# Kernel optimization log

Hardware: AMD Instinct MI355X
Metric: run time of the kernel (lower is better)

Reference implementation:

```python
import jax, jax.numpy as jnp
import numpy as np

B, T, E, R, A, M = 64, 2000, 512, 1024, 512, 8


def setup_inputs() -> dict:
    key = jax.random.key(0)
    ks = jax.random.split(key, 9)
    attention_hidden_state = jax.random.normal(ks[0], (B, R), dtype=jnp.float32)
    memory = jax.random.normal(ks[1], (B, T, E), dtype=jnp.float32)
    previous_location = jax.random.uniform(ks[2], (B, 1, M), dtype=jnp.float32) * 10.0
    mask = jnp.zeros((B, T), dtype=bool)
    # F = Linear(R->A, bias, xavier tanh) -> Linear(A->A, no bias, xavier tanh) -> tanh -> lin(A->3M, bias)
    g = 5.0 / 3.0  # tanh gain
    lim1 = g * np.sqrt(6.0 / (R + A))
    W1 = jax.random.uniform(ks[3], (A, R), minval=-lim1, maxval=lim1, dtype=jnp.float32)
    b1 = jnp.zeros((A,), dtype=jnp.float32)
    lim2 = g * np.sqrt(6.0 / (A + A))
    W2 = jax.random.uniform(ks[4], (A, A), minval=-lim2, maxval=lim2, dtype=jnp.float32)
    lim3 = np.sqrt(1.0 / A)
    Wlin = jax.random.uniform(ks[5], (3 * M, A), minval=-lim3, maxval=lim3, dtype=jnp.float32) * 0.01
    blin = jax.random.uniform(ks[6], (3 * M,), minval=-lim3, maxval=lim3, dtype=jnp.float32) * 0.008 - 2.0
    return {"attention_hidden_state": attention_hidden_state, "memory": memory,
            "previous_location": previous_location, "mask": mask,
            "W1": W1, "b1": b1, "W2": W2, "Wlin": Wlin, "blin": blin}


def reference(attention_hidden_state, memory, previous_location, mask, W1, b1, W2, Wlin, blin):
    # normalize_attention_input=True
    h = jnp.tanh(attention_hidden_state)                       # (B, R)
    x = jnp.tanh((h @ W1.T + b1) @ W2.T)                       # (B, A) 2-layer variant
    y = (x @ Wlin.T + blin)[:, None, :]                        # (B, 1, 3M)
    m = y.shape[-1] // 3
    w, delta, scale = y[..., :m], y[..., m:2 * m], y[..., 2 * m:]
    delta = jax.nn.sigmoid(delta)                              # (B, 1, M)
    loc = previous_location + delta                            # (B, 1, M)
    scale = jax.nn.sigmoid(scale) * 2.0 + 1.0                  # (B, 1, M)
    pos = jnp.arange(memory.shape[1], dtype=memory.dtype)[None, :, None]  # (1, T, 1)
    d = loc - pos                                              # (B, T, M)
    z = 0.5 * (jax.lax.erf((d + 0.5) * scale) - jax.lax.erf((d - 0.5) * scale))
    wmix = jax.nn.sigmoid(w)[:, 0, :]                          # (B, M)
    alignment = jnp.einsum('btm,bm->bt', z, wmix)              # (B, T)
    alignment = jnp.where(mask, jnp.zeros((), alignment.dtype), alignment)  # score_mask_value=0
    attention_weights = jax.nn.softmax(alignment, axis=1)      # (B, T)
    attention_context = jnp.einsum('bt,bte->be', attention_weights, memory)  # (B, E)
    return attention_context, attention_weights, loc
```

## Files before the change

kernel.cpp:

```cpp
#include <hip/hip_runtime.h>
#include <math.h>

#define B 64
#define T 2000
#define E 512
#define R 1024
#define A 512
#define M 8

#define NCH 16
#define TCH (T / NCH)

__device__ __forceinline__ float sigmoidf_(float x) { return 1.0f / (1.0f + expf(-x)); }

__global__ __launch_bounds__(512) void mlp_align_kernel(
    const float* __restrict__ ahs, const float* __restrict__ prev_loc,
    const unsigned char* __restrict__ mask,
    const float* __restrict__ W1, const float* __restrict__ b1,
    const float* __restrict__ W2, const float* __restrict__ Wlin,
    const float* __restrict__ blin,
    float* __restrict__ out_w,
    float* __restrict__ out_loc)
{
    __shared__ float sh_h[R];
    __shared__ float sh_t[A];
    __shared__ float sh_x[A];
    __shared__ float sh_y[3 * M];
    __shared__ float sh_wmix[M], sh_loc[M], sh_scale[M];
    __shared__ float sred[8];
    __shared__ float sbval;

    const int b = blockIdx.x;
    const int tid = threadIdx.x;

    for (int k = tid; k < R; k += 512) sh_h[k] = tanhf(ahs[b * R + k]);
    __syncthreads();

    {
        const int j = tid;
        const float4* w4 = (const float4*)(W1 + (size_t)j * R);
        const float4* h4 = (const float4*)sh_h;
        float a0 = 0.f, a1 = 0.f, a2 = 0.f, a3 = 0.f;
#pragma unroll 4
        for (int k4 = 0; k4 < R / 4; k4 += 4) {
            float4 x0 = h4[k4 + 0], w0 = w4[k4 + 0];
            float4 x1 = h4[k4 + 1], w1 = w4[k4 + 1];
            float4 x2 = h4[k4 + 2], w2 = w4[k4 + 2];
            float4 x3 = h4[k4 + 3], w3 = w4[k4 + 3];
            a0 += x0.x * w0.x + x0.y * w0.y + x0.z * w0.z + x0.w * w0.w;
            a1 += x1.x * w1.x + x1.y * w1.y + x1.z * w1.z + x1.w * w1.w;
            a2 += x2.x * w2.x + x2.y * w2.y + x2.z * w2.z + x2.w * w2.w;
            a3 += x3.x * w3.x + x3.y * w3.y + x3.z * w3.z + x3.w * w3.w;
        }
        sh_t[j] = (a0 + a1) + (a2 + a3) + b1[j];
    }
    __syncthreads();

    {
        const int j = tid;
        const float4* w4 = (const float4*)(W2 + (size_t)j * A);
        const float4* t4 = (const float4*)sh_t;
        float a0 = 0.f, a1 = 0.f, a2 = 0.f, a3 = 0.f;
#pragma unroll 4
        for (int k4 = 0; k4 < A / 4; k4 += 4) {
            float4 x0 = t4[k4 + 0], w0 = w4[k4 + 0];
            float4 x1 = t4[k4 + 1], w1 = w4[k4 + 1];
            float4 x2 = t4[k4 + 2], w2 = w4[k4 + 2];
            float4 x3 = t4[k4 + 3], w3 = w4[k4 + 3];
            a0 += x0.x * w0.x + x0.y * w0.y + x0.z * w0.z + x0.w * w0.w;
            a1 += x1.x * w1.x + x1.y * w1.y + x1.z * w1.z + x1.w * w1.w;
            a2 += x2.x * w2.x + x2.y * w2.y + x2.z * w2.z + x2.w * w2.w;
            a3 += x3.x * w3.x + x3.y * w3.y + x3.z * w3.z + x3.w * w3.w;
        }
        sh_x[j] = tanhf((a0 + a1) + (a2 + a3));
    }
    __syncthreads();

    if (tid < 16 * 3 * M) {
        const int i = tid >> 4;
        const int lane = tid & 15;
        float s = 0.f;
        for (int k = lane; k < A; k += 16) s += sh_x[k] * Wlin[i * A + k];
        s += __shfl_down(s, 8, 16);
        s += __shfl_down(s, 4, 16);
        s += __shfl_down(s, 2, 16);
        s += __shfl_down(s, 1, 16);
        if (lane == 0) sh_y[i] = s + blin[i];
    }
    __syncthreads();

    if (tid < M) {
        const int m = tid;
        const float delta = sigmoidf_(sh_y[M + m]);
        const float loc = prev_loc[b * M + m] + delta;
        sh_wmix[m]  = sigmoidf_(sh_y[m]);
        sh_loc[m]   = loc;
        sh_scale[m] = sigmoidf_(sh_y[2 * M + m]) * 2.0f + 1.0f;
        out_loc[b * M + m] = loc;
    }
    __syncthreads();

    float a[4];
    float lmax = -1e30f;
#pragma unroll
    for (int i = 0; i < 4; ++i) {
        const int t = tid + i * 512;
        float v = 0.f;
        if (t < T) {
            const float tf = (float)t;
#pragma unroll
            for (int m = 0; m < M; ++m) {
                const float d = sh_loc[m] - tf;
                const float s = sh_scale[m];
                v += 0.5f * (erff((d + 0.5f) * s) - erff((d - 0.5f) * s)) * sh_wmix[m];
            }
            if (mask[b * T + t]) v = 0.f;
            lmax = fmaxf(lmax, v);
        }
        a[i] = v;
    }

    for (int off = 32; off > 0; off >>= 1) lmax = fmaxf(lmax, __shfl_down(lmax, off));
    if ((tid & 63) == 0) sred[tid >> 6] = lmax;
    __syncthreads();
    if (tid == 0) {
        float m0 = sred[0];
        for (int i = 1; i < 8; ++i) m0 = fmaxf(m0, sred[i]);
        sbval = m0;
    }
    __syncthreads();
    const float bmax = sbval;

    float lsum = 0.f;
#pragma unroll
    for (int i = 0; i < 4; ++i) {
        const int t = tid + i * 512;
        if (t < T) {
            a[i] = expf(a[i] - bmax);
            lsum += a[i];
        }
    }
    for (int off = 32; off > 0; off >>= 1) lsum += __shfl_down(lsum, off);
    if ((tid & 63) == 0) sred[tid >> 6] = lsum;
    __syncthreads();
    if (tid == 0) {
        float s0 = 0.f;
        for (int i = 0; i < 8; ++i) s0 += sred[i];
        sbval = s0;
    }
    __syncthreads();
    const float inv = 1.0f / sbval;

#pragma unroll
    for (int i = 0; i < 4; ++i) {
        const int t = tid + i * 512;
        if (t < T) out_w[b * T + t] = a[i] * inv;
    }
}

__global__ __launch_bounds__(512) void context_partial_kernel(
    const float* __restrict__ memory,
    const float* __restrict__ w,
    float* __restrict__ partials)
{
    __shared__ float sh_w[TCH];
    __shared__ float4 sh_acc[512];

    const int b = blockIdx.x;
    const int chunk = blockIdx.y;
    const int tid = threadIdx.x;
    const int t0 = chunk * TCH;

    if (tid < TCH) sh_w[tid] = w[b * T + t0 + tid];
    __syncthreads();

    const int e4 = tid & 127;
    const int tp = tid >> 7;
    const float4* mem4 = (const float4*)(memory + (size_t)(b * T + t0) * E);

    float4 acc = {0.f, 0.f, 0.f, 0.f};
#pragma unroll 4
    for (int t = tp; t < TCH; t += 4) {
        const float wv = sh_w[t];
        const float4 mv = mem4[(size_t)t * (E / 4) + e4];
        acc.x += wv * mv.x;
        acc.y += wv * mv.y;
        acc.z += wv * mv.z;
        acc.w += wv * mv.w;
    }
    sh_acc[tid] = acc;
    __syncthreads();

    if (tid < 128) {
        const float4 a0 = sh_acc[tid];
        const float4 a1 = sh_acc[tid + 128];
        const float4 a2 = sh_acc[tid + 256];
        const float4 a3 = sh_acc[tid + 384];
        float4 r;
        r.x = (a0.x + a1.x) + (a2.x + a3.x);
        r.y = (a0.y + a1.y) + (a2.y + a3.y);
        r.z = (a0.z + a1.z) + (a2.z + a3.z);
        r.w = (a0.w + a1.w) + (a2.w + a3.w);
        float4* dst = (float4*)(partials + ((size_t)b * NCH + chunk) * E);
        dst[tid] = r;
    }
}

__global__ __launch_bounds__(256) void context_reduce_kernel(
    const float* __restrict__ partials,
    float* __restrict__ out_ctx)
{
    const int idx = blockIdx.x * 256 + threadIdx.x;
    const int b = idx >> 9;
    const int e = idx & (E - 1);
    float s = 0.f;
#pragma unroll
    for (int c = 0; c < NCH; ++c) s += partials[((size_t)b * NCH + c) * E + e];
    out_ctx[idx] = s;
}

extern "C" void kernel_launch(void* const* d_in, const int* in_sizes, int n_in,
                              void* d_out, int out_size, void* d_ws, size_t ws_size,
                              hipStream_t stream) {
    const float* ahs      = (const float*)d_in[0];
    const float* memory   = (const float*)d_in[1];
    const float* prev_loc = (const float*)d_in[2];
    const unsigned char* mask = (const unsigned char*)d_in[3];
    const float* W1   = (const float*)d_in[4];
    const float* b1   = (const float*)d_in[5];
    const float* W2   = (const float*)d_in[6];
    const float* Wlin = (const float*)d_in[7];
    const float* blin = (const float*)d_in[8];

    float* out = (float*)d_out;
    float* out_ctx = out;
    float* out_w   = out + B * E;
    float* out_loc = out + B * E + B * T;
    float* partials = (float*)d_ws;

    mlp_align_kernel<<<dim3(B), dim3(512), 0, stream>>>(
        ahs, prev_loc, mask, W1, b1, W2, Wlin, blin, out_w, out_loc);

    context_partial_kernel<<<dim3(B, NCH), dim3(512), 0, stream>>>(
        memory, out_w, partials);

    context_reduce_kernel<<<dim3((B * E) / 256), dim3(256), 0, stream>>>(
        partials, out_ctx);
}
```

Before: 478.6 us.

## Coalesce MLP weight reads, drop softmax max pass, stream memory nontemporally

The MLP matvecs now use one wave per output row, so consecutive lanes read a row with coalesced float4 loads and a shuffle reduces it, replacing the strided per-thread row reads. The softmax max-subtraction pass and one block reduction are removed, since the alignment values are bounded mixture weights. The context partial kernel uses nontemporal loads and writes four partials per chunk without a shared-memory reduction, and the final reduce kernel is vectorised with float4 over 64 partials. Risks: skipping the max subtraction assumes small logits, and the workspace holds four times as many partials.

```diff
diff --git a/kernel.cpp b/kernel.cpp
--- a/kernel.cpp
+++ b/kernel.cpp
@@ -10,8 +10,14 @@
 
 #define NCH 16
 #define TCH (T / NCH)
+#define NP  (NCH * 4)
+
+typedef float nfloat4 __attribute__((ext_vector_type(4)));
 
 __device__ __forceinline__ float sigmoidf_(float x) { return 1.0f / (1.0f + expf(-x)); }
+__device__ __forceinline__ float dot4_(float4 a, float4 b) {
+    return (a.x * b.x + a.y * b.y) + (a.z * b.z + a.w * b.w);
+}
 
 __global__ __launch_bounds__(512) void mlp_align_kernel(
     const float* __restrict__ ahs, const float* __restrict__ prev_loc,
@@ -32,60 +38,73 @@
 
     const int b = blockIdx.x;
     const int tid = threadIdx.x;
+    const int wave = tid >> 6;
+    const int lane = tid & 63;
 
     for (int k = tid; k < R; k += 512) sh_h[k] = tanhf(ahs[b * R + k]);
     __syncthreads();
 
     {
-        const int j = tid;
-        const float4* w4 = (const float4*)(W1 + (size_t)j * R);
         const float4* h4 = (const float4*)sh_h;
-        float a0 = 0.f, a1 = 0.f, a2 = 0.f, a3 = 0.f;
-#pragma unroll 4
-        for (int k4 = 0; k4 < R / 4; k4 += 4) {
-            float4 x0 = h4[k4 + 0], w0 = w4[k4 + 0];
-            float4 x1 = h4[k4 + 1], w1 = w4[k4 + 1];
-            float4 x2 = h4[k4 + 2], w2 = w4[k4 + 2];
-            float4 x3 = h4[k4 + 3], w3 = w4[k4 + 3];
-            a0 += x0.x * w0.x + x0.y * w0.y + x0.z * w0.z + x0.w * w0.w;
-            a1 += x1.x * w1.x + x1.y * w1.y + x1.z * w1.z + x1.w * w1.w;
-            a2 += x2.x * w2.x + x2.y * w2.y + x2.z * w2.z + x2.w * w2.w;
-            a3 += x3.x * w3.x + x3.y * w3.y + x3.z * w3.z + x3.w * w3.w;
+        const float4 h0 = h4[lane], h1 = h4[lane + 64],
+                     h2 = h4[lane + 128], h3 = h4[lane + 192];
+        for (int j = 0; j < 64; j += 2) {
+            const int ja = wave * 64 + j;
+            const int jb = ja + 1;
+            const float4* ra = (const float4*)(W1 + (size_t)ja * R);
+            const float4* rb = (const float4*)(W1 + (size_t)jb * R);
+            float4 a0 = ra[lane], a1 = ra[lane + 64], a2 = ra[lane + 128], a3 = ra[lane + 192];
+            float4 c0 = rb[lane], c1 = rb[lane + 64], c2 = rb[lane + 128], c3 = rb[lane + 192];
+            float accA = (dot4_(h0, a0) + dot4_(h1, a1)) + (dot4_(h2, a2) + dot4_(h3, a3));
+            float accB = (dot4_(h0, c0) + dot4_(h1, c1)) + (dot4_(h2, c2) + dot4_(h3, c3));
+#pragma unroll
+            for (int off = 32; off > 0; off >>= 1) {
+                accA += __shfl_down(accA, off);
+                accB += __shfl_down(accB, off);
+            }
+            if (lane == 0) {
+                sh_t[ja] = accA + b1[ja];
+                sh_t[jb] = accB + b1[jb];
+            }
         }
-        sh_t[j] = (a0 + a1) + (a2 + a3) + b1[j];
     }
     __syncthreads();
 
     {
-        const int j = tid;
-        const float4* w4 = (const float4*)(W2 + (size_t)j * A);
         const float4* t4 = (const float4*)sh_t;
-        float a0 = 0.f, a1 = 0.f, a2 = 0.f, a3 = 0.f;
-#pragma unroll 4
-        for (int k4 = 0; k4 < A / 4; k4 += 4) {
-            float4 x0 = t4[k4 + 0], w0 = w4[k4 + 0];
-            float4 x1 = t4[k4 + 1], w1 = w4[k4 + 1];
-            float4 x2 = t4[k4 + 2], w2 = w4[k4 + 2];
-            float4 x3 = t4[k4 + 3], w3 = w4[k4 + 3];
-            a0 += x0.x * w0.x + x0.y * w0.y + x0.z * w0.z + x0.w * w0.w;
-            a1 += x1.x * w1.x + x1.y * w1.y + x1.z * w1.z + x1.w * w1.w;
-            a2 += x2.x * w2.x + x2.y * w2.y + x2.z * w2.z + x2.w * w2.w;
-            a3 += x3.x * w3.x + x3.y * w3.y + x3.z * w3.z + x3.w * w3.w;
+        const float4 t0 = t4[lane], t1 = t4[lane + 64];
+        for (int j = 0; j < 64; j += 2) {
+            const int ja = wave * 64 + j;
+            const int jb = ja + 1;
+            const float4* ra = (const float4*)(W2 + (size_t)ja * A);
+            const float4* rb = (const float4*)(W2 + (size_t)jb * A);
+            float4 a0 = ra[lane], a1 = ra[lane + 64];
+            float4 c0 = rb[lane], c1 = rb[lane + 64];
+            float accA = dot4_(t0, a0) + dot4_(t1, a1);
+            float accB = dot4_(t0, c0) + dot4_(t1, c1);
+#pragma unroll
+            for (int off = 32; off > 0; off >>= 1) {
+                accA += __shfl_down(accA, off);
+                accB += __shfl_down(accB, off);
+            }
+            if (lane == 0) {
+                sh_x[ja] = tanhf(accA);
+                sh_x[jb] = tanhf(accB);
+            }
         }
-        sh_x[j] = tanhf((a0 + a1) + (a2 + a3));
     }
     __syncthreads();
 
     if (tid < 16 * 3 * M) {
         const int i = tid >> 4;
-        const int lane = tid & 15;
+        const int l16 = tid & 15;
         float s = 0.f;
-        for (int k = lane; k < A; k += 16) s += sh_x[k] * Wlin[i * A + k];
+        for (int k = l16; k < A; k += 16) s += sh_x[k] * Wlin[i * A + k];
         s += __shfl_down(s, 8, 16);
         s += __shfl_down(s, 4, 16);
         s += __shfl_down(s, 2, 16);
         s += __shfl_down(s, 1, 16);
-        if (lane == 0) sh_y[i] = s + blin[i];
+        if (l16 == 0) sh_y[i] = s + blin[i];
     }
     __syncthreads();
 
@@ -101,13 +120,13 @@
     __syncthreads();
 
     float a[4];
-    float lmax = -1e30f;
+    float lsum = 0.f;
 #pragma unroll
     for (int i = 0; i < 4; ++i) {
         const int t = tid + i * 512;
-        float v = 0.f;
         if (t < T) {
             const float tf = (float)t;
+            float v = 0.f;
 #pragma unroll
             for (int m = 0; m < M; ++m) {
                 const float d = sh_loc[m] - tf;
@@ -115,33 +134,15 @@
                 v += 0.5f * (erff((d + 0.5f) * s) - erff((d - 0.5f) * s)) * sh_wmix[m];
             }
             if (mask[b * T + t]) v = 0.f;
-            lmax = fmaxf(lmax, v);
+            a[i] = expf(v);
+            lsum += a[i];
+        } else {
+            a[i] = 0.f;
         }
-        a[i] = v;
-    }
-
-    for (int off = 32; off > 0; off >>= 1) lmax = fmaxf(lmax, __shfl_down(lmax, off));
-    if ((tid & 63) == 0) sred[tid >> 6] = lmax;
-    __syncthreads();
-    if (tid == 0) {
-        float m0 = sred[0];
-        for (int i = 1; i < 8; ++i) m0 = fmaxf(m0, sred[i]);
-        sbval = m0;
-    }
-    __syncthreads();
-    const float bmax = sbval;
-
-    float lsum = 0.f;
-#pragma unroll
-    for (int i = 0; i < 4; ++i) {
-        const int t = tid + i * 512;
-        if (t < T) {
-            a[i] = expf(a[i] - bmax);
-            lsum += a[i];
-        }
-    }
+    }
+#pragma unroll
     for (int off = 32; off > 0; off >>= 1) lsum += __shfl_down(lsum, off);
-    if ((tid & 63) == 0) sred[tid >> 6] = lsum;
+    if (lane == 0) sred[wave] = lsum;
     __syncthreads();
     if (tid == 0) {
         float s0 = 0.f;
@@ -164,7 +165,6 @@
     float* __restrict__ partials)
 {
     __shared__ float sh_w[TCH];
-    __shared__ float4 sh_acc[512];
 
     const int b = blockIdx.x;
     const int chunk = blockIdx.y;
@@ -176,34 +176,22 @@
 
     const int e4 = tid & 127;
     const int tp = tid >> 7;
-    const float4* mem4 = (const float4*)(memory + (size_t)(b * T + t0) * E);
-
-    float4 acc = {0.f, 0.f, 0.f, 0.f};
+    const nfloat4* mem4 = (const nfloat4*)(memory + (size_t)(b * T + t0) * E);
+
+    float acc0 = 0.f, acc1 = 0.f, acc2 = 0.f, acc3 = 0.f;
 #pragma unroll 4
     for (int t = tp; t < TCH; t += 4) {
         const float wv = sh_w[t];
-        const float4 mv = mem4[(size_t)t * (E / 4) + e4];
-        acc.x += wv * mv.x;
-        acc.y += wv * mv.y;
-        acc.z += wv * mv.z;
-        acc.w += wv * mv.w;
-    }
-    sh_acc[tid] = acc;
-    __syncthreads();
-
-    if (tid < 128) {
-        const float4 a0 = sh_acc[tid];
-        const float4 a1 = sh_acc[tid + 128];
-        const float4 a2 = sh_acc[tid + 256];
-        const float4 a3 = sh_acc[tid + 384];
-        float4 r;
-        r.x = (a0.x + a1.x) + (a2.x + a3.x);
-        r.y = (a0.y + a1.y) + (a2.y + a3.y);
-        r.z = (a0.z + a1.z) + (a2.z + a3.z);
-        r.w = (a0.w + a1.w) + (a2.w + a3.w);
-        float4* dst = (float4*)(partials + ((size_t)b * NCH + chunk) * E);
-        dst[tid] = r;
-    }
+        const nfloat4 mv = __builtin_nontemporal_load(&mem4[(size_t)t * (E / 4) + e4]);
+        acc0 += wv * mv.x;
+        acc1 += wv * mv.y;
+        acc2 += wv * mv.z;
+        acc3 += wv * mv.w;
+    }
+
+    nfloat4 accv = {acc0, acc1, acc2, acc3};
+    nfloat4* dst = (nfloat4*)(partials + (((size_t)b * NCH + chunk) * 4 + tp) * E);
+    dst[e4] = accv;
 }
 
 __global__ __launch_bounds__(256) void context_reduce_kernel(
@@ -211,12 +199,16 @@
     float* __restrict__ out_ctx)
 {
     const int idx = blockIdx.x * 256 + threadIdx.x;
-    const int b = idx >> 9;
-    const int e = idx & (E - 1);
-    float s = 0.f;
-#pragma unroll
-    for (int c = 0; c < NCH; ++c) s += partials[((size_t)b * NCH + c) * E + e];
-    out_ctx[idx] = s;
+    const int b = idx >> 7;
+    const int e4 = idx & 127;
+    const float4* p = (const float4*)partials + (size_t)b * NP * (E / 4) + e4;
+    float4 s = {0.f, 0.f, 0.f, 0.f};
+#pragma unroll 8
+    for (int c = 0; c < NP; ++c) {
+        const float4 v = p[(size_t)c * (E / 4)];
+        s.x += v.x; s.y += v.y; s.z += v.z; s.w += v.w;
+    }
+    ((float4*)out_ctx)[idx] = s;
 }
 
 extern "C" void kernel_launch(void* const* d_in, const int* in_sizes, int n_in,
@@ -244,6 +236,6 @@
     context_partial_kernel<<<dim3(B, NCH), dim3(512), 0, stream>>>(
         memory, out_w, partials);
 
-    context_reduce_kernel<<<dim3((B * E) / 256), dim3(256), 0, stream>>>(
+    context_reduce_kernel<<<dim3((B * E / 4) / 256), dim3(256), 0, stream>>>(
         partials, out_ctx);
 }
```

Result: faster. 434.3 us (-9.3%).
